# Optimization experiments

Hardware: AMD Instinct MI355X
Metric: run time of the kernel (lower is better)

The kernel has to match this reference:

```python
import jax, jax.numpy as jnp
import numpy as np

B, N, F, E, D, H, L = 4, 2048, 2, 16, 32, 4, 2
GRAPH_LAYERS = 3
FLOW_ITERS = 10
COST_C = 1.0        # quadratic cost: c*x^2, inv_derivative(y) = y/(2c)
BIG_NUMBER = 1e7


def setup_inputs():
    key = jax.random.key(0)
    ks = jax.random.split(key, 20)
    node_features = jax.random.normal(ks[0], (B, N, F), jnp.float32)
    node_embeddings = jax.random.normal(ks[1], (B, N, E), jnp.float32)
    demands = jax.random.normal(ks[2], (B, N, 1), jnp.float32)
    demands = demands - demands.mean(axis=1, keepdims=True)  # flow conservation
    adj = (jax.random.uniform(ks[3], (B, N, N)) < 0.01).astype(jnp.float32)
    adj = adj * (1.0 - jnp.eye(N, dtype=jnp.float32))
    eye = jnp.broadcast_to(jnp.eye(N, dtype=jnp.float32), (B, N, N))
    neighborhoods = jnp.stack([eye, adj], axis=1)  # [B,L,N,N] hop-0 and hop-1
    def g(k, shape):
        return jax.random.normal(k, shape, jnp.float32) * 0.1
    params = {
        'We1': g(ks[4], (E + F, D)), 'be1': jnp.zeros((D,), jnp.float32),
        'We2': g(ks[5], (D, D)), 'be2': jnp.zeros((D,), jnp.float32),
        'w_attn': g(ks[6], (H, D)),
        'Wo': g(ks[7], (D, D)), 'bo': jnp.zeros((D,), jnp.float32),
        'Wz': g(ks[8], (D, D)), 'Uz': g(ks[9], (D, D)), 'bz': jnp.zeros((D,), jnp.float32),
        'Wr': g(ks[10], (D, D)), 'Ur': g(ks[11], (D, D)), 'br': jnp.zeros((D,), jnp.float32),
        'Wh': g(ks[12], (D, D)), 'Uh': g(ks[13], (D, D)), 'bh': jnp.zeros((D,), jnp.float32),
        'Wd1': g(ks[14], (D, D)), 'bd1': jnp.zeros((D,), jnp.float32),
        'Wd2': g(ks[15], (D, 1)), 'bd2': jnp.zeros((1,), jnp.float32),
        'Wv1': g(ks[16], (D, D)), 'bv1': jnp.zeros((D,), jnp.float32),
        'Wv2': g(ks[17], (D, 1)), 'bv2': jnp.zeros((1,), jnp.float32),
    }
    return {'node_features': node_features, 'node_embeddings': node_embeddings,
            'demands': demands, 'adj': adj, 'neighborhoods': neighborhoods, **params}


def _forward(node_features, node_embeddings, demands, adj, neighborhoods,
             We1, be1, We2, be2, w_attn, Wo, bo,
             Wz, Uz, bz, Wr, Ur, br, Wh, Uh, bh,
             Wd1, bd1, Wd2, bd2, Wv1, bv1, Wv2, bv2):
    # --- node encoder MLP (tanh, activate_final=True) ---
    x = jnp.concatenate([node_embeddings, node_features], axis=-1)   # [B,N,E+F]
    enc = jnp.tanh(jnp.tanh(x @ We1 + be1) @ We2 + be2)               # [B,N,D]
    # row-normalized neighborhood operators (degree-normalized aggregation)
    Mnorm = neighborhoods / (jnp.sum(neighborhoods, axis=-1, keepdims=True) + 1.0)
    # --- graph_layers x (attention neighborhood + GRU state update) ---
    for _ in range(GRAPH_LAYERS):
        agg = jnp.einsum('blnm,bmd->blnd', Mnorm, enc)                # [B,L,N,D]
        scores = jnp.einsum('blnd,hd->bhnl', jnp.tanh(agg), w_attn)   # [B,H,N,L]
        alpha = jax.nn.softmax(scores, axis=-1)
        ctx = jnp.einsum('bhnl,blnd->bnd', alpha, agg) / H            # mean over heads
        nbr = jnp.tanh(ctx @ Wo + bo)                                 # [B,N,D]
        z = jax.nn.sigmoid(nbr @ Wz + enc @ Uz + bz)
        r = jax.nn.sigmoid(nbr @ Wr + enc @ Ur + br)
        h = jnp.tanh(nbr @ Wh + (r * enc) @ Uh + bh)
        enc = z * enc + (1.0 - z) * h
    # --- primal: edge weights, masked softmax, proportional flow solver ---
    pred = (enc @ Wd1 + bd1) @ Wd2 + bd2                              # [B,N,1]
    pw = pred * jnp.transpose(pred, (0, 2, 1))                        # [B,N,N]
    weights = -BIG_NUMBER * (1.0 - adj) + pw
    fwp = jax.nn.softmax(weights, axis=-1)                            # rows sum to 1
    flow0 = fwp * jax.nn.relu(-demands)

    def step(flow, _):
        inflow = jnp.sum(flow, axis=1)[..., None]                     # [B,N,1]
        return fwp * jax.nn.relu(inflow - demands), None

    flow, _ = jax.lax.scan(step, flow0, None, length=FLOW_ITERS)
    flow_cost = jnp.sum(COST_C * flow * flow, axis=(1, 2))            # [B]
    # --- dual: dual variables, dual flows via inverse cost derivative ---
    dual = (enc @ Wv1 + bv1) @ Wv2 + bv2                              # [B,N,1]
    dd = dual - jnp.transpose(dual, (0, 2, 1))                        # [B,N,N]
    df = adj * jax.nn.relu(dd / (2.0 * COST_C))
    dual_cost = jnp.sum(COST_C * df * df - dd * df, axis=(1, 2)) \
        - jnp.sum(dual * demands, axis=(1, 2))                        # [B]
    return flow_cost - dual_cost                                      # primal-dual gap loss, [B]


def reference(node_features, node_embeddings, demands, adj, neighborhoods,
              We1, be1, We2, be2, w_attn, Wo, bo,
              Wz, Uz, bz, Wr, Ur, br, Wh, Uh, bh,
              Wd1, bd1, Wd2, bd2, Wv1, bv1, Wv2, bv2):
    return _forward(node_features, node_embeddings, demands, adj, neighborhoods,
                    We1, be1, We2, be2, w_attn, Wo, bo,
                    Wz, Uz, bz, Wr, Ur, br, Wh, Uh, bh,
                    Wd1, bd1, Wd2, bd2, Wv1, bv1, Wv2, bv2)
```

## Files before the change

kernel.cpp:

```cpp
#include <hip/hip_runtime.h>

#define NN 2048
#define NB 4
#define BN (NB * NN)
#define MAXD 96

__global__ __launch_bounds__(256) void k_encoder(
    const float* __restrict__ feat, const float* __restrict__ emb,
    const float* __restrict__ We1, const float* __restrict__ be1,
    const float* __restrict__ We2, const float* __restrict__ be2,
    float* __restrict__ enc_out)
{
    __shared__ float sW1[18 * 32], sb1[32], sW2[32 * 32], sb2[32];
    int tid = threadIdx.x;
    for (int i = tid; i < 18 * 32; i += 256) sW1[i] = We1[i];
    for (int i = tid; i < 32 * 32; i += 256) sW2[i] = We2[i];
    if (tid < 32) { sb1[tid] = be1[tid]; sb2[tid] = be2[tid]; }
    __syncthreads();
    int group = tid >> 5, j = tid & 31;
    int node = blockIdx.x * 8 + group;
    float x;
    if (j < 16)      x = emb[node * 16 + j];
    else if (j < 18) x = feat[node * 2 + (j - 16)];
    else             x = 0.f;
    float acc = sb1[j];
#pragma unroll
    for (int k = 0; k < 18; k++)
        acc += __shfl(x, k, 32) * sW1[k * 32 + j];
    float h = tanhf(acc);
    float acc2 = sb2[j];
#pragma unroll
    for (int k = 0; k < 32; k++)
        acc2 += __shfl(h, k, 32) * sW2[k * 32 + j];
    enc_out[node * 32 + j] = tanhf(acc2);
}

__global__ __launch_bounds__(256) void k_build(
    const float* __restrict__ adj, int* __restrict__ deg, int* __restrict__ cols)
{
    int wave = threadIdx.x >> 6, lane = threadIdx.x & 63;
    int row = blockIdx.x * 4 + wave;
    const float4* p = (const float4*)(adj + (size_t)row * NN);
    int cnt = 0;
    int base = row * MAXD;
#pragma unroll
    for (int it = 0; it < 8; it++) {
        float4 v = p[it * 64 + lane];
        float va[4] = { v.x, v.y, v.z, v.w };
#pragma unroll
        for (int c = 0; c < 4; c++) {
            unsigned long long m = __ballot(va[c] != 0.f);
            if (va[c] != 0.f) {
                int pos = cnt + __popcll(m & ((1ull << lane) - 1ull));
                if (pos < MAXD) cols[base + pos] = it * 256 + lane * 4 + c;
            }
            cnt += __popcll(m);
        }
    }
    if (lane == 0) deg[row] = cnt < MAXD ? cnt : MAXD;
}

__global__ __launch_bounds__(256) void k_layer(
    const float* __restrict__ enc_in, float* __restrict__ enc_out,
    const int* __restrict__ deg, const int* __restrict__ cols,
    const float* __restrict__ w_attn,
    const float* __restrict__ Wo, const float* __restrict__ bo,
    const float* __restrict__ Wz, const float* __restrict__ Uz, const float* __restrict__ bz,
    const float* __restrict__ Wr, const float* __restrict__ Ur, const float* __restrict__ br,
    const float* __restrict__ Wh, const float* __restrict__ Uh, const float* __restrict__ bh)
{
    __shared__ float sWo[1024], sWz[1024], sUz[1024], sWr[1024], sUr[1024], sWh[1024], sUh[1024];
    __shared__ float sbo[32], sbz[32], sbr[32], sbh[32], sAttn[128];
    int tid = threadIdx.x;
    for (int i = tid; i < 1024; i += 256) {
        sWo[i] = Wo[i]; sWz[i] = Wz[i]; sUz[i] = Uz[i];
        sWr[i] = Wr[i]; sUr[i] = Ur[i]; sWh[i] = Wh[i]; sUh[i] = Uh[i];
    }
    if (tid < 32) { sbo[tid] = bo[tid]; sbz[tid] = bz[tid]; sbr[tid] = br[tid]; sbh[tid] = bh[tid]; }
    if (tid < 128) sAttn[tid] = w_attn[tid];
    __syncthreads();
    int group = tid >> 5, j = tid & 31;
    int node = blockIdx.x * 8 + group;
    int b = node >> 11;
    const float* encB = enc_in + (size_t)(b * NN) * 32;
    float e = enc_in[node * 32 + j];
    float agg0 = 0.5f * e;
    int d = deg[node];
    const int* cp = cols + node * MAXD;
    float a1 = 0.f;
    for (int i = 0; i < d; i++) {
        int m = cp[i];
        a1 += encB[m * 32 + j];
    }
    a1 *= 1.0f / (float)(d + 1);
    float t0 = tanhf(agg0), t1 = tanhf(a1);
    float sc[8];
#pragma unroll
    for (int h2 = 0; h2 < 4; h2++) { sc[h2] = sAttn[h2 * 32 + j] * t0; sc[4 + h2] = sAttn[h2 * 32 + j] * t1; }
#pragma unroll
    for (int off = 16; off >= 1; off >>= 1)
#pragma unroll
        for (int q = 0; q < 8; q++) sc[q] += __shfl_xor(sc[q], off, 32);
    float c0 = 0.f, c1 = 0.f;
#pragma unroll
    for (int h2 = 0; h2 < 4; h2++) {
        float a = sc[h2], bsc = sc[4 + h2];
        float mx = fmaxf(a, bsc);
        float e0 = expf(a - mx), e1 = expf(bsc - mx);
        float inv = 1.0f / (e0 + e1);
        c0 += e0 * inv; c1 += e1 * inv;
    }
    c0 *= 0.25f; c1 *= 0.25f;
    float ctx = c0 * agg0 + c1 * a1;
    float acc = sbo[j];
#pragma unroll
    for (int k = 0; k < 32; k++) acc += __shfl(ctx, k, 32) * sWo[k * 32 + j];
    float nbr = tanhf(acc);
    float az = sbz[j], ar = sbr[j], ah = sbh[j];
#pragma unroll
    for (int k = 0; k < 32; k++) {
        float nb = __shfl(nbr, k, 32);
        float en = __shfl(e, k, 32);
        az += nb * sWz[k * 32 + j] + en * sUz[k * 32 + j];
        ar += nb * sWr[k * 32 + j] + en * sUr[k * 32 + j];
        ah += nb * sWh[k * 32 + j];
    }
    float z = 1.0f / (1.0f + expf(-az));
    float r = 1.0f / (1.0f + expf(-ar));
    float re = r * e;
#pragma unroll
    for (int k = 0; k < 32; k++) ah += __shfl(re, k, 32) * sUh[k * 32 + j];
    float hc = tanhf(ah);
    enc_out[node * 32 + j] = z * e + (1.0f - z) * hc;
}

__global__ __launch_bounds__(256) void k_heads(
    const float* __restrict__ enc,
    const float* __restrict__ Wd1, const float* __restrict__ bd1,
    const float* __restrict__ Wd2, const float* __restrict__ bd2,
    const float* __restrict__ Wv1, const float* __restrict__ bv1,
    const float* __restrict__ Wv2, const float* __restrict__ bv2,
    float* __restrict__ pred, float* __restrict__ dual)
{
    __shared__ float sWd1[1024], sWv1[1024], sbd1[32], sbv1[32], sWd2[32], sWv2[32];
    int tid = threadIdx.x;
    for (int i = tid; i < 1024; i += 256) { sWd1[i] = Wd1[i]; sWv1[i] = Wv1[i]; }
    if (tid < 32) { sbd1[tid] = bd1[tid]; sbv1[tid] = bv1[tid]; sWd2[tid] = Wd2[tid]; sWv2[tid] = Wv2[tid]; }
    __syncthreads();
    int group = tid >> 5, j = tid & 31;
    int node = blockIdx.x * 8 + group;
    float e = enc[node * 32 + j];
    float ad = sbd1[j], av = sbv1[j];
#pragma unroll
    for (int k = 0; k < 32; k++) {
        float en = __shfl(e, k, 32);
        ad += en * sWd1[k * 32 + j];
        av += en * sWv1[k * 32 + j];
    }
    float pd = ad * sWd2[j];
    float dv = av * sWv2[j];
#pragma unroll
    for (int off = 16; off >= 1; off >>= 1) {
        pd += __shfl_xor(pd, off, 32);
        dv += __shfl_xor(dv, off, 32);
    }
    if (j == 0) { pred[node] = pd + bd2[0]; dual[node] = dv + bv2[0]; }
}

__global__ __launch_bounds__(256) void k_edge_softmax(
    const int* __restrict__ deg, const int* __restrict__ cols,
    const float* __restrict__ pred, const float* __restrict__ dual,
    float* __restrict__ fwp, float* __restrict__ rowsq, float* __restrict__ rowdual)
{
    int wave = threadIdx.x >> 6, lane = threadIdx.x & 63;
    int row = blockIdx.x * 4 + wave;
    int b = row >> 11;
    const float* predB = pred + b * NN;
    const float* dualB = dual + b * NN;
    int d = deg[row];
    int base = row * MAXD;
    float pn = pred[row];
    float dn = dual[row];
    float mx = -1e30f;
    for (int i = lane; i < d; i += 64) {
        int c = cols[base + i];
        mx = fmaxf(mx, pn * predB[c]);
    }
#pragma unroll
    for (int off = 32; off >= 1; off >>= 1) mx = fmaxf(mx, __shfl_xor(mx, off));
    float den = 0.f, du = 0.f;
    for (int i = lane; i < d; i += 64) {
        int c = cols[base + i];
        den += expf(pn * predB[c] - mx);
        float dd = dn - dualB[c];
        if (dd > 0.f) du -= 0.25f * dd * dd;
    }
#pragma unroll
    for (int off = 32; off >= 1; off >>= 1) { den += __shfl_xor(den, off); du += __shfl_xor(du, off); }
    float invden = 1.0f / den;
    float rs = 0.f;
    for (int i = lane; i < d; i += 64) {
        int c = cols[base + i];
        float f = expf(pn * predB[c] - mx) * invden;
        fwp[base + i] = f;
        rs += f * f;
    }
#pragma unroll
    for (int off = 32; off >= 1; off >>= 1) rs += __shfl_xor(rs, off);
    if (lane == 0) { rowsq[row] = rs; rowdual[row] = du; }
}

__global__ __launch_bounds__(256) void k_pre(
    const float* __restrict__ demands, int* __restrict__ tdeg, float* __restrict__ s0)
{
    int n = blockIdx.x * 256 + threadIdx.x;
    tdeg[n] = 0;
    s0[n] = fmaxf(-demands[n], 0.f);
}

__global__ __launch_bounds__(256) void k_transpose(
    const int* __restrict__ deg, const int* __restrict__ cols,
    const float* __restrict__ fwp,
    int* __restrict__ tdeg, int* __restrict__ tcols, float* __restrict__ tvals)
{
    int wave = threadIdx.x >> 6, lane = threadIdx.x & 63;
    int row = blockIdx.x * 4 + wave;
    int b = row >> 11;
    int rloc = row & (NN - 1);
    int d = deg[row];
    int base = row * MAXD;
    for (int i = lane; i < d; i += 64) {
        int c = cols[base + i];
        float f = fwp[base + i];
        int tgt = b * NN + c;
        int pos = atomicAdd(&tdeg[tgt], 1);
        if (pos < MAXD) {
            tcols[pos * BN + tgt] = rloc;
            tvals[pos * BN + tgt] = f;
        }
    }
}

__global__ __launch_bounds__(64) void k_flow_iter(
    const int* __restrict__ tdeg, const int* __restrict__ tcols,
    const float* __restrict__ tvals, const float* __restrict__ demands,
    const float* __restrict__ s_in, float* __restrict__ s_out)
{
    int n = blockIdx.x * 64 + threadIdx.x;
    const float* sB = s_in + (n & ~(NN - 1));
    int d = tdeg[n];
    float acc = 0.f;
#pragma unroll 4
    for (int i = 0; i < d; i++) {
        acc += tvals[i * BN + n] * sB[tcols[i * BN + n]];
    }
    s_out[n] = fmaxf(acc - demands[n], 0.f);
}

__global__ __launch_bounds__(256) void k_finish(
    const float* __restrict__ s_fin, const float* __restrict__ demands,
    const float* __restrict__ rowsq, const float* __restrict__ rowdual,
    const float* __restrict__ dual, float* __restrict__ out)
{
    __shared__ float red[3][4];
    int tid = threadIdx.x;
    int b = blockIdx.x;
    float fc = 0.f, ds = 0.f, dq = 0.f;
    for (int n = tid; n < NN; n += 256) {
        int row = b * NN + n;
        float sv = s_fin[row];
        fc += rowsq[row] * sv * sv;
        ds += rowdual[row];
        dq += dual[row] * demands[row];
    }
#pragma unroll
    for (int off = 32; off >= 1; off >>= 1) {
        fc += __shfl_xor(fc, off);
        ds += __shfl_xor(ds, off);
        dq += __shfl_xor(dq, off);
    }
    int wv = tid >> 6;
    if ((tid & 63) == 0) { red[0][wv] = fc; red[1][wv] = ds; red[2][wv] = dq; }
    __syncthreads();
    if (tid == 0) {
        float a = 0.f, bb = 0.f, cc = 0.f;
        for (int w = 0; w < 4; w++) { a += red[0][w]; bb += red[1][w]; cc += red[2][w]; }
        out[b] = a - bb + cc;
    }
}

extern "C" void kernel_launch(void* const* d_in, const int* in_sizes, int n_in,
                              void* d_out, int out_size, void* d_ws, size_t ws_size,
                              hipStream_t stream) {
    const float* feat = (const float*)d_in[0];
    const float* emb  = (const float*)d_in[1];
    const float* dem  = (const float*)d_in[2];
    const float* adj  = (const float*)d_in[3];
    const float* We1 = (const float*)d_in[5];
    const float* be1 = (const float*)d_in[6];
    const float* We2 = (const float*)d_in[7];
    const float* be2 = (const float*)d_in[8];
    const float* w_attn = (const float*)d_in[9];
    const float* Wo = (const float*)d_in[10];
    const float* bo = (const float*)d_in[11];
    const float* Wz = (const float*)d_in[12];
    const float* Uz = (const float*)d_in[13];
    const float* bz = (const float*)d_in[14];
    const float* Wr = (const float*)d_in[15];
    const float* Ur = (const float*)d_in[16];
    const float* br = (const float*)d_in[17];
    const float* Wh = (const float*)d_in[18];
    const float* Uh = (const float*)d_in[19];
    const float* bh = (const float*)d_in[20];
    const float* Wd1 = (const float*)d_in[21];
    const float* bd1 = (const float*)d_in[22];
    const float* Wd2 = (const float*)d_in[23];
    const float* bd2 = (const float*)d_in[24];
    const float* Wv1 = (const float*)d_in[25];
    const float* bv1 = (const float*)d_in[26];
    const float* Wv2 = (const float*)d_in[27];
    const float* bv2 = (const float*)d_in[28];
    float* out = (float*)d_out;

    float* w = (float*)d_ws;
    float* enc0 = w;            w += (size_t)BN * 32;
    float* enc1 = w;            w += (size_t)BN * 32;
    int*   degp = (int*)w;      w += BN;
    int*   colp = (int*)w;      w += (size_t)BN * MAXD;
    float* fwpp = w;            w += (size_t)BN * MAXD;
    float* pred = w;            w += BN;
    float* dual = w;            w += BN;
    float* rowsq = w;           w += BN;
    float* rowdual = w;         w += BN;
    int*   tdeg = (int*)w;      w += BN;
    int*   tcol = (int*)w;      w += (size_t)BN * MAXD;
    float* tval = w;            w += (size_t)BN * MAXD;
    float* sA = w;              w += BN;
    float* sB = w;              w += BN;

    k_encoder<<<BN / 8, 256, 0, stream>>>(feat, emb, We1, be1, We2, be2, enc0);
    k_build<<<BN / 4, 256, 0, stream>>>(adj, degp, colp);
    k_layer<<<BN / 8, 256, 0, stream>>>(enc0, enc1, degp, colp, w_attn,
                                        Wo, bo, Wz, Uz, bz, Wr, Ur, br, Wh, Uh, bh);
    k_layer<<<BN / 8, 256, 0, stream>>>(enc1, enc0, degp, colp, w_attn,
                                        Wo, bo, Wz, Uz, bz, Wr, Ur, br, Wh, Uh, bh);
    k_layer<<<BN / 8, 256, 0, stream>>>(enc0, enc1, degp, colp, w_attn,
                                        Wo, bo, Wz, Uz, bz, Wr, Ur, br, Wh, Uh, bh);
    k_heads<<<BN / 8, 256, 0, stream>>>(enc1, Wd1, bd1, Wd2, bd2, Wv1, bv1, Wv2, bv2, pred, dual);
    k_edge_softmax<<<BN / 4, 256, 0, stream>>>(degp, colp, pred, dual, fwpp, rowsq, rowdual);
    k_pre<<<BN / 256, 256, 0, stream>>>(dem, tdeg, sA);
    k_transpose<<<BN / 4, 256, 0, stream>>>(degp, colp, fwpp, tdeg, tcol, tval);
    for (int it = 0; it < 10; it++) {
        const float* si = (it & 1) ? sB : sA;
        float* so = (it & 1) ? sA : sB;
        k_flow_iter<<<BN / 64, 64, 0, stream>>>(tdeg, tcol, tval, dem, si, so);
    }
    k_finish<<<NB, 256, 0, stream>>>(sA, dem, rowsq, rowdual, dual, out);
}
```

Before: 454.7 us.

## Fuse front kernels, merge softmax with transpose, and run flow iterations persistently

Merges the encoder and adjacency-build kernels into one launch, and folds the k_pre initialisation into the build and head kernels. It also merges edge softmax with the transpose scatter, which removes the fwp intermediate buffer. The ten flow iterations and the final reduction move into one persistent 32-block kernel that uses a global atomic barrier, replacing eleven small launches. This cuts launch overhead and intermediate traffic, but the flow phase now runs on only 32 blocks and depends on all of them being co-resident for the spin barrier.

```diff
diff --git a/kernel.cpp b/kernel.cpp
--- a/kernel.cpp
+++ b/kernel.cpp
@@ -4,60 +4,65 @@
 #define NB 4
 #define BN (NB * NN)
 #define MAXD 96
-
-__global__ __launch_bounds__(256) void k_encoder(
+#define FBLK 32
+
+__global__ __launch_bounds__(256) void k_front(
     const float* __restrict__ feat, const float* __restrict__ emb,
     const float* __restrict__ We1, const float* __restrict__ be1,
     const float* __restrict__ We2, const float* __restrict__ be2,
-    float* __restrict__ enc_out)
-{
-    __shared__ float sW1[18 * 32], sb1[32], sW2[32 * 32], sb2[32];
+    float* __restrict__ enc_out,
+    const float* __restrict__ adj, int* __restrict__ deg, int* __restrict__ cols,
+    int* __restrict__ tdeg, int* __restrict__ barcnt)
+{
     int tid = threadIdx.x;
-    for (int i = tid; i < 18 * 32; i += 256) sW1[i] = We1[i];
-    for (int i = tid; i < 32 * 32; i += 256) sW2[i] = We2[i];
-    if (tid < 32) { sb1[tid] = be1[tid]; sb2[tid] = be2[tid]; }
-    __syncthreads();
-    int group = tid >> 5, j = tid & 31;
-    int node = blockIdx.x * 8 + group;
-    float x;
-    if (j < 16)      x = emb[node * 16 + j];
-    else if (j < 18) x = feat[node * 2 + (j - 16)];
-    else             x = 0.f;
-    float acc = sb1[j];
-#pragma unroll
-    for (int k = 0; k < 18; k++)
-        acc += __shfl(x, k, 32) * sW1[k * 32 + j];
-    float h = tanhf(acc);
-    float acc2 = sb2[j];
-#pragma unroll
-    for (int k = 0; k < 32; k++)
-        acc2 += __shfl(h, k, 32) * sW2[k * 32 + j];
-    enc_out[node * 32 + j] = tanhf(acc2);
-}
-
-__global__ __launch_bounds__(256) void k_build(
-    const float* __restrict__ adj, int* __restrict__ deg, int* __restrict__ cols)
-{
-    int wave = threadIdx.x >> 6, lane = threadIdx.x & 63;
-    int row = blockIdx.x * 4 + wave;
-    const float4* p = (const float4*)(adj + (size_t)row * NN);
-    int cnt = 0;
-    int base = row * MAXD;
-#pragma unroll
-    for (int it = 0; it < 8; it++) {
-        float4 v = p[it * 64 + lane];
-        float va[4] = { v.x, v.y, v.z, v.w };
-#pragma unroll
-        for (int c = 0; c < 4; c++) {
-            unsigned long long m = __ballot(va[c] != 0.f);
-            if (va[c] != 0.f) {
-                int pos = cnt + __popcll(m & ((1ull << lane) - 1ull));
-                if (pos < MAXD) cols[base + pos] = it * 256 + lane * 4 + c;
+    if (blockIdx.x < 1024) {
+        __shared__ float sW1[18 * 32], sb1[32], sW2[32 * 32], sb2[32];
+        for (int i = tid; i < 18 * 32; i += 256) sW1[i] = We1[i];
+        for (int i = tid; i < 32 * 32; i += 256) sW2[i] = We2[i];
+        if (tid < 32) { sb1[tid] = be1[tid]; sb2[tid] = be2[tid]; }
+        __syncthreads();
+        int group = tid >> 5, j = tid & 31;
+        int node = blockIdx.x * 8 + group;
+        float x;
+        if (j < 16)      x = emb[node * 16 + j];
+        else if (j < 18) x = feat[node * 2 + (j - 16)];
+        else             x = 0.f;
+        float acc = sb1[j];
+#pragma unroll
+        for (int k = 0; k < 18; k++)
+            acc += __shfl(x, k, 32) * sW1[k * 32 + j];
+        float h = tanhf(acc);
+        float acc2 = sb2[j];
+#pragma unroll
+        for (int k = 0; k < 32; k++)
+            acc2 += __shfl(h, k, 32) * sW2[k * 32 + j];
+        enc_out[node * 32 + j] = tanhf(acc2);
+    } else {
+        if (blockIdx.x == 1024 && tid == 0) barcnt[0] = 0;
+        int wave = tid >> 6, lane = tid & 63;
+        int row = (blockIdx.x - 1024) * 4 + wave;
+        const float4* p = (const float4*)(adj + (size_t)row * NN);
+        int cnt = 0;
+        int base = row * MAXD;
+#pragma unroll
+        for (int it = 0; it < 8; it++) {
+            float4 v = p[it * 64 + lane];
+            float va[4] = { v.x, v.y, v.z, v.w };
+#pragma unroll
+            for (int c = 0; c < 4; c++) {
+                unsigned long long m = __ballot(va[c] != 0.f);
+                if (va[c] != 0.f) {
+                    int pos = cnt + __popcll(m & ((1ull << lane) - 1ull));
+                    if (pos < MAXD) cols[base + pos] = it * 256 + lane * 4 + c;
+                }
+                cnt += __popcll(m);
             }
-            cnt += __popcll(m);
-        }
-    }
-    if (lane == 0) deg[row] = cnt < MAXD ? cnt : MAXD;
+        }
+        if (lane == 0) {
+            deg[row] = cnt < MAXD ? cnt : MAXD;
+            tdeg[row] = 0;
+        }
+    }
 }
 
 __global__ __launch_bounds__(256) void k_layer(
@@ -135,12 +140,12 @@
 }
 
 __global__ __launch_bounds__(256) void k_heads(
-    const float* __restrict__ enc,
+    const float* __restrict__ enc, const float* __restrict__ demands,
     const float* __restrict__ Wd1, const float* __restrict__ bd1,
     const float* __restrict__ Wd2, const float* __restrict__ bd2,
     const float* __restrict__ Wv1, const float* __restrict__ bv1,
     const float* __restrict__ Wv2, const float* __restrict__ bv2,
-    float* __restrict__ pred, float* __restrict__ dual)
+    float* __restrict__ pred, float* __restrict__ dual, float* __restrict__ s0)
 {
     __shared__ float sWd1[1024], sWv1[1024], sbd1[32], sbv1[32], sWd2[32], sWv2[32];
     int tid = threadIdx.x;
@@ -164,17 +169,23 @@
         pd += __shfl_xor(pd, off, 32);
         dv += __shfl_xor(dv, off, 32);
     }
-    if (j == 0) { pred[node] = pd + bd2[0]; dual[node] = dv + bv2[0]; }
-}
-
-__global__ __launch_bounds__(256) void k_edge_softmax(
+    if (j == 0) {
+        pred[node] = pd + bd2[0];
+        dual[node] = dv + bv2[0];
+        s0[node] = fmaxf(-demands[node], 0.f);
+    }
+}
+
+__global__ __launch_bounds__(256) void k_edge_scatter(
     const int* __restrict__ deg, const int* __restrict__ cols,
     const float* __restrict__ pred, const float* __restrict__ dual,
-    float* __restrict__ fwp, float* __restrict__ rowsq, float* __restrict__ rowdual)
+    int* __restrict__ tdeg, int* __restrict__ tcols, float* __restrict__ tvals,
+    float* __restrict__ rowsq, float* __restrict__ rowdual)
 {
     int wave = threadIdx.x >> 6, lane = threadIdx.x & 63;
     int row = blockIdx.x * 4 + wave;
     int b = row >> 11;
+    int rloc = row & (NN - 1);
     const float* predB = pred + b * NN;
     const float* dualB = dual + b * NN;
     int d = deg[row];
@@ -202,36 +213,7 @@
     for (int i = lane; i < d; i += 64) {
         int c = cols[base + i];
         float f = expf(pn * predB[c] - mx) * invden;
-        fwp[base + i] = f;
         rs += f * f;
-    }
-#pragma unroll
-    for (int off = 32; off >= 1; off >>= 1) rs += __shfl_xor(rs, off);
-    if (lane == 0) { rowsq[row] = rs; rowdual[row] = du; }
-}
-
-__global__ __launch_bounds__(256) void k_pre(
-    const float* __restrict__ demands, int* __restrict__ tdeg, float* __restrict__ s0)
-{
-    int n = blockIdx.x * 256 + threadIdx.x;
-    tdeg[n] = 0;
-    s0[n] = fmaxf(-demands[n], 0.f);
-}
-
-__global__ __launch_bounds__(256) void k_transpose(
-    const int* __restrict__ deg, const int* __restrict__ cols,
-    const float* __restrict__ fwp,
-    int* __restrict__ tdeg, int* __restrict__ tcols, float* __restrict__ tvals)
-{
-    int wave = threadIdx.x >> 6, lane = threadIdx.x & 63;
-    int row = blockIdx.x * 4 + wave;
-    int b = row >> 11;
-    int rloc = row & (NN - 1);
-    int d = deg[row];
-    int base = row * MAXD;
-    for (int i = lane; i < d; i += 64) {
-        int c = cols[base + i];
-        float f = fwp[base + i];
         int tgt = b * NN + c;
         int pos = atomicAdd(&tdeg[tgt], 1);
         if (pos < MAXD) {
@@ -239,53 +221,69 @@
             tvals[pos * BN + tgt] = f;
         }
     }
-}
-
-__global__ __launch_bounds__(64) void k_flow_iter(
+#pragma unroll
+    for (int off = 32; off >= 1; off >>= 1) rs += __shfl_xor(rs, off);
+    if (lane == 0) { rowsq[row] = rs; rowdual[row] = du; }
+}
+
+__global__ __launch_bounds__(256) void k_flow_persist(
     const int* __restrict__ tdeg, const int* __restrict__ tcols,
     const float* __restrict__ tvals, const float* __restrict__ demands,
-    const float* __restrict__ s_in, float* __restrict__ s_out)
-{
-    int n = blockIdx.x * 64 + threadIdx.x;
-    const float* sB = s_in + (n & ~(NN - 1));
-    int d = tdeg[n];
-    float acc = 0.f;
-#pragma unroll 4
-    for (int i = 0; i < d; i++) {
-        acc += tvals[i * BN + n] * sB[tcols[i * BN + n]];
-    }
-    s_out[n] = fmaxf(acc - demands[n], 0.f);
-}
-
-__global__ __launch_bounds__(256) void k_finish(
-    const float* __restrict__ s_fin, const float* __restrict__ demands,
+    float* __restrict__ sA, float* __restrict__ sB,
     const float* __restrict__ rowsq, const float* __restrict__ rowdual,
-    const float* __restrict__ dual, float* __restrict__ out)
+    const float* __restrict__ dual,
+    int* __restrict__ barcnt, float* __restrict__ out)
 {
     __shared__ float red[3][4];
     int tid = threadIdx.x;
-    int b = blockIdx.x;
-    float fc = 0.f, ds = 0.f, dq = 0.f;
-    for (int n = tid; n < NN; n += 256) {
-        int row = b * NN + n;
-        float sv = s_fin[row];
-        fc += rowsq[row] * sv * sv;
-        ds += rowdual[row];
-        dq += dual[row] * demands[row];
-    }
-#pragma unroll
-    for (int off = 32; off >= 1; off >>= 1) {
-        fc += __shfl_xor(fc, off);
-        ds += __shfl_xor(ds, off);
-        dq += __shfl_xor(dq, off);
-    }
-    int wv = tid >> 6;
-    if ((tid & 63) == 0) { red[0][wv] = fc; red[1][wv] = ds; red[2][wv] = dq; }
-    __syncthreads();
-    if (tid == 0) {
-        float a = 0.f, bb = 0.f, cc = 0.f;
-        for (int w = 0; w < 4; w++) { a += red[0][w]; bb += red[1][w]; cc += red[2][w]; }
-        out[b] = a - bb + cc;
+    int n = blockIdx.x * 256 + tid;
+    int bb = n & ~(NN - 1);
+    int d = tdeg[n];
+    float dm = demands[n];
+    float* bufs[2] = { sA, sB };
+    for (int it = 0; it < 10; it++) {
+        const float* si = bufs[it & 1] + bb;
+        float* so = bufs[(it & 1) ^ 1];
+        float acc = 0.f;
+        for (int i = 0; i < d; i++) {
+            acc += tvals[i * BN + n] * si[tcols[i * BN + n]];
+        }
+        so[n] = fmaxf(acc - dm, 0.f);
+        __threadfence();
+        __syncthreads();
+        if (tid == 0) {
+            __hip_atomic_fetch_add(barcnt, 1, __ATOMIC_RELEASE, __HIP_MEMORY_SCOPE_AGENT);
+            int target = FBLK * (it + 1);
+            while (__hip_atomic_load(barcnt, __ATOMIC_ACQUIRE, __HIP_MEMORY_SCOPE_AGENT) < target)
+                __builtin_amdgcn_s_sleep(2);
+        }
+        __syncthreads();
+        __threadfence();
+    }
+    if (blockIdx.x < NB) {
+        int b = blockIdx.x;
+        float fc = 0.f, ds = 0.f, dq = 0.f;
+        for (int k = tid; k < NN; k += 256) {
+            int row = b * NN + k;
+            float sv = sA[row];
+            fc += rowsq[row] * sv * sv;
+            ds += rowdual[row];
+            dq += dual[row] * demands[row];
+        }
+#pragma unroll
+        for (int off = 32; off >= 1; off >>= 1) {
+            fc += __shfl_xor(fc, off);
+            ds += __shfl_xor(ds, off);
+            dq += __shfl_xor(dq, off);
+        }
+        int wv = tid >> 6;
+        if ((tid & 63) == 0) { red[0][wv] = fc; red[1][wv] = ds; red[2][wv] = dq; }
+        __syncthreads();
+        if (tid == 0) {
+            float a = 0.f, s1 = 0.f, s2 = 0.f;
+            for (int w = 0; w < 4; w++) { a += red[0][w]; s1 += red[1][w]; s2 += red[2][w]; }
+            out[b] = a - s1 + s2;
+        }
     }
 }
 
@@ -327,7 +325,6 @@
     float* enc1 = w;            w += (size_t)BN * 32;
     int*   degp = (int*)w;      w += BN;
     int*   colp = (int*)w;      w += (size_t)BN * MAXD;
-    float* fwpp = w;            w += (size_t)BN * MAXD;
     float* pred = w;            w += BN;
     float* dual = w;            w += BN;
     float* rowsq = w;           w += BN;
@@ -337,23 +334,20 @@
     float* tval = w;            w += (size_t)BN * MAXD;
     float* sA = w;              w += BN;
     float* sB = w;              w += BN;
-
-    k_encoder<<<BN / 8, 256, 0, stream>>>(feat, emb, We1, be1, We2, be2, enc0);
-    k_build<<<BN / 4, 256, 0, stream>>>(adj, degp, colp);
+    int*   barcnt = (int*)w;    w += 64;
+
+    k_front<<<3072, 256, 0, stream>>>(feat, emb, We1, be1, We2, be2, enc0,
+                                      adj, degp, colp, tdeg, barcnt);
     k_layer<<<BN / 8, 256, 0, stream>>>(enc0, enc1, degp, colp, w_attn,
                                         Wo, bo, Wz, Uz, bz, Wr, Ur, br, Wh, Uh, bh);
     k_layer<<<BN / 8, 256, 0, stream>>>(enc1, enc0, degp, colp, w_attn,
                                         Wo, bo, Wz, Uz, bz, Wr, Ur, br, Wh, Uh, bh);
     k_layer<<<BN / 8, 256, 0, stream>>>(enc0, enc1, degp, colp, w_attn,
                                         Wo, bo, Wz, Uz, bz, Wr, Ur, br, Wh, Uh, bh);
-    k_heads<<<BN / 8, 256, 0, stream>>>(enc1, Wd1, bd1, Wd2, bd2, Wv1, bv1, Wv2, bv2, pred, dual);
-    k_edge_softmax<<<BN / 4, 256, 0, stream>>>(degp, colp, pred, dual, fwpp, rowsq, rowdual);
-    k_pre<<<BN / 256, 256, 0, stream>>>(dem, tdeg, sA);
-    k_transpose<<<BN / 4, 256, 0, stream>>>(degp, colp, fwpp, tdeg, tcol, tval);
-    for (int it = 0; it < 10; it++) {
-        const float* si = (it & 1) ? sB : sA;
-        float* so = (it & 1) ? sA : sB;
-        k_flow_iter<<<BN / 64, 64, 0, stream>>>(tdeg, tcol, tval, dem, si, so);
-    }
-    k_finish<<<NB, 256, 0, stream>>>(sA, dem, rowsq, rowdual, dual, out);
-}
+    k_heads<<<BN / 8, 256, 0, stream>>>(enc1, dem, Wd1, bd1, Wd2, bd2, Wv1, bv1, Wv2, bv2,
+                                        pred, dual, sA);
+    k_edge_scatter<<<BN / 4, 256, 0, stream>>>(degp, colp, pred, dual,
+                                               tdeg, tcol, tval, rowsq, rowdual);
+    k_flow_persist<<<FBLK, 256, 0, stream>>>(tdeg, tcol, tval, dem, sA, sB,
+                                             rowsq, rowdual, dual, barcnt, out);
+}
```

Measured after the change: 552.0 us. 21.4% more time.
